# Performance work log

Hardware: AMD Instinct MI355X
Metric: run time of the kernel (lower is better)

## Reference

```python
import jax, jax.numpy as jnp
import numpy as np

N, E, F0, H = 100000, 3200000, 256, 128
TEMP = 2.0
ALPHA = 0.2  # leaky relu slope
EPS_BN = 1e-5
EPS_LN = 1e-5


def spmm(vals, row, col, X):
    # sparse [N,N] @ dense [N,D] via gather + segment_sum
    return jax.ops.segment_sum(vals[:, None] * X[col], row, num_segments=N)


def batchnorm(h, g, b):
    mu = jnp.mean(h, axis=0, keepdims=True)
    var = jnp.var(h, axis=0, keepdims=True)
    return (h - mu) * jax.lax.rsqrt(var + EPS_BN) * g + b


def layernorm(h, g, b):
    mu = jnp.mean(h, axis=-1, keepdims=True)
    var = jnp.var(h, axis=-1, keepdims=True)
    return (h - mu) * jax.lax.rsqrt(var + EPS_LN) * g + b


def setup_inputs() -> dict:
    key = jax.random.key(0)
    ks = jax.random.split(key, 32)
    x = jax.random.normal(ks[0], (N, F0), dtype=jnp.float32)
    edge_row = jax.random.randint(ks[1], (E,), 0, N)
    edge_col = jax.random.randint(ks[2], (E,), 0, N)
    adj_vals = jax.random.uniform(ks[3], (E,), dtype=jnp.float32) / 32.0  # ~normalized adj
    sf = lambda k, sh: jax.random.normal(k, sh, dtype=jnp.float32) * 0.05
    in_dim = 3 * F0 + 1
    return {
        "x": x, "edge_row": edge_row, "edge_col": edge_col, "adj_vals": adj_vals,
        # LowPassExtractor (GCN)
        "W_gc1": sf(ks[4], (F0, 2 * H)), "b_gc1": jnp.zeros((2 * H,), jnp.float32),
        "bn1_g": jnp.ones((2 * H,), jnp.float32), "bn1_b": jnp.zeros((2 * H,), jnp.float32),
        "W_gc2": sf(ks[5], (2 * H, H)), "b_gc2": jnp.zeros((H,), jnp.float32),
        "bn2_g": jnp.ones((H,), jnp.float32), "bn2_b": jnp.zeros((H,), jnp.float32),
        # Gating
        "Wg1": sf(ks[6], (in_dim, H)), "bg1": jnp.zeros((H,), jnp.float32),
        "ln_g": jnp.ones((H,), jnp.float32), "ln_b": jnp.zeros((H,), jnp.float32),
        "Wg2": sf(ks[7], (H, 2)), "bg2": jnp.zeros((2,), jnp.float32),
        # HighPassExpert
        "Wxp": sf(ks[8], (F0, H)), "bxp": jnp.zeros((H,), jnp.float32),
        "res_scale": jnp.asarray(1.0, jnp.float32),
        "rn_g": jnp.ones((H,), jnp.float32), "rn_b": jnp.zeros((H,), jnp.float32),
        "Wq": sf(ks[9], (H, H)), "Wk": sf(ks[10], (H, H)), "Wv": sf(ks[11], (H, H)),
    }


def reference(x, edge_row, edge_col, adj_vals,
              W_gc1, b_gc1, bn1_g, bn1_b, W_gc2, b_gc2, bn2_g, bn2_b,
              Wg1, bg1, ln_g, ln_b, Wg2, bg2,
              Wxp, bxp, res_scale, rn_g, rn_b, Wq, Wk, Wv):
    # ---- LowPassExtractor: two GCN layers (spmm(adj, xW)+b) with batchnorm+relu
    h1 = jax.nn.relu(batchnorm(spmm(adj_vals, edge_row, edge_col, x @ W_gc1) + b_gc1, bn1_g, bn1_b))
    low = jax.nn.relu(batchnorm(spmm(adj_vals, edge_row, edge_col, h1 @ W_gc2) + b_gc2, bn2_g, bn2_b))

    # ---- Gating: neighborhood stats via spmm
    AX = spmm(adj_vals, edge_row, edge_col, x)
    deg = jax.ops.segment_sum(adj_vals, edge_row, num_segments=N)[:, None]
    x_mean = AX / (deg + 1e-8)
    AX2 = spmm(adj_vals, edge_row, edge_col, x * x)
    var = AX2 / (deg + 1e-8) - x_mean * x_mean
    x_std = jnp.sqrt(jnp.clip(var, 0.0))
    x_cat = jnp.concatenate([x, AX - x, x_std, deg], axis=1)  # [N, 3*F0+1]
    hg = jax.nn.relu(layernorm(x_cat @ Wg1 + bg1, ln_g, ln_b))
    gate = jax.nn.softmax((hg @ Wg2 + bg2) / TEMP, axis=1)  # [N, 2]

    # ---- HighPassExpert: GAT-style sparse attention on normalized residual
    residual = layernorm(res_scale * (x @ Wxp + bxp - low), rn_g, rn_b)
    Q, K, V = residual @ Wq, residual @ Wk, residual @ Wv
    scores = jnp.sum(Q[edge_row] * K[edge_col], axis=1) / jnp.sqrt(jnp.float32(H))
    exp_s = jnp.exp(jnp.where(scores > 0, scores, ALPHA * scores))
    denom = jax.ops.segment_sum(exp_s, edge_row, num_segments=N)
    attn = exp_s / (denom[edge_row] + 1e-16)
    high = jax.ops.segment_sum(attn[:, None] * V[edge_col], edge_row, num_segments=N)

    output = gate[:, 0:1] * low + gate[:, 1:2] * high
    return output, gate, low, high
```

## Files before the change

kernel.cpp:

```cpp
#include <hip/hip_runtime.h>

#define F0 256
#define HD 128
#define NP 100352

typedef unsigned short u16;
typedef __attribute__((ext_vector_type(8))) short short8;
typedef __attribute__((ext_vector_type(4))) float f32x4;

__device__ inline float bf2f(u16 u) {
    union { unsigned int i; float f; } v; v.i = ((unsigned int)u) << 16; return v.f;
}
__device__ inline u16 f2bf(float f) {
    union { float f; unsigned int i; } v; v.f = f;
    unsigned int r = v.i + 0x7FFF + ((v.i >> 16) & 1);
    return (u16)(r >> 16);
}

#define GLOAD16(gp, lp) __builtin_amdgcn_global_load_lds( \
    (const __attribute__((address_space(1))) void*)(gp), \
    (__attribute__((address_space(3))) void*)(lp), 16, 0, 0)

__global__ void k_hist(const int* __restrict__ row, int* __restrict__ counts, int E) {
    int e = blockIdx.x * blockDim.x + threadIdx.x;
    if (e < E) atomicAdd(&counts[row[e]], 1);
}

__global__ void k_scan_blk(const int* __restrict__ counts, int* __restrict__ scan_out,
                           int* __restrict__ partials, int n) {
    __shared__ int wsum[16];
    int t = threadIdx.x;
    int i = blockIdx.x * 1024 + t;
    int v = (i < n) ? counts[i] : 0;
    int lane = t & 63, w = t >> 6;
    #pragma unroll
    for (int off = 1; off < 64; off <<= 1) { int u = __shfl_up(v, off); if (lane >= off) v += u; }
    if (lane == 63) wsum[w] = v;
    __syncthreads();
    if (t < 16) {
        int s = wsum[t];
        #pragma unroll
        for (int off = 1; off < 16; off <<= 1) { int u = __shfl_up(s, off); if (t >= off) s += u; }
        wsum[t] = s;
    }
    __syncthreads();
    int add = (w > 0) ? wsum[w - 1] : 0;
    if (i < n) scan_out[i] = v + add;
    if (t == 1023) partials[blockIdx.x] = wsum[15];
}

__global__ void k_scan_part(int* partials, int nb) {
    __shared__ int ws2[2];
    int t = threadIdx.x;
    int v = (t < nb) ? partials[t] : 0;
    int lane = t & 63, w = t >> 6;
    #pragma unroll
    for (int off = 1; off < 64; off <<= 1) { int u = __shfl_up(v, off); if (lane >= off) v += u; }
    if (lane == 63) ws2[w] = v;
    __syncthreads();
    if (w == 1) v += ws2[0];
    if (t < nb) partials[t] = v;
}

__global__ void k_scan_add(int* __restrict__ row_ptr, const int* __restrict__ partials, int n) {
    int b = blockIdx.x;
    int i = b * 1024 + threadIdx.x;
    if (b == 0 && threadIdx.x == 0) row_ptr[0] = 0;
    int add = (b > 0) ? partials[b - 1] : 0;
    if (i < n) row_ptr[1 + i] += add;
}

__global__ void k_scatter_cv(const int* __restrict__ row, const int* __restrict__ ecol,
                             const float* __restrict__ avals, const int* __restrict__ row_ptr,
                             int* __restrict__ cursor, int2* __restrict__ cv, int E) {
    int e = blockIdx.x * blockDim.x + threadIdx.x;
    if (e >= E) return;
    int r = row[e];
    int pos = row_ptr[r] + atomicAdd(&cursor[r], 1);
    cv[pos] = make_int2(ecol[e], __float_as_int(avals[e]));
}

__global__ void k_cast_x(const float* __restrict__ x, u16* __restrict__ xb, int total4) {
    int i = blockIdx.x * blockDim.x + threadIdx.x;
    if (i >= total4) return;
    float4 v = ((const float4*)x)[i];
    ((ushort4*)xb)[i] = make_ushort4(f2bf(v.x), f2bf(v.y), f2bf(v.z), f2bf(v.w));
}

__global__ void k_prep_w(const float* __restrict__ W_gc1, const float* __restrict__ W_gc2,
                         const float* __restrict__ Wg1, const float* __restrict__ Wxp,
                         const float* __restrict__ Wq, const float* __restrict__ Wk,
                         const float* __restrict__ Wv,
                         u16* Wgc1t, u16* Wgc2t, u16* Wdt, u16* W1t, u16* W2t,
                         u16* Wxpt, u16* Wqt, u16* Wkt, u16* Wvt) {
    int z = blockIdx.z;
    int idx = blockIdx.x * 256 + threadIdx.x;
    if (z == 0) { if (idx < 65536) { int n = idx >> 8, k = idx & 255; Wgc1t[idx] = f2bf(W_gc1[k * 256 + n]); } }
    else if (z == 1) { if (idx < 32768) { int n = idx >> 8, k = idx & 255; Wgc2t[idx] = f2bf(W_gc2[k * 128 + n]); } }
    else if (z == 2) { if (idx < 32768) { int n = idx >> 8, k = idx & 255; Wdt[idx] = f2bf(Wg1[k * 128 + n] - Wg1[(k + 256) * 128 + n]); } }
    else if (z == 3) { if (idx < 32768) { int n = idx >> 8, k = idx & 255; W1t[idx] = f2bf(Wg1[(k + 256) * 128 + n]); } }
    else if (z == 4) { if (idx < 32768) { int n = idx >> 8, k = idx & 255; W2t[idx] = f2bf(Wg1[(k + 512) * 128 + n]); } }
    else if (z == 5) { if (idx < 32768) { int n = idx >> 8, k = idx & 255; Wxpt[idx] = f2bf(Wxp[k * 128 + n]); } }
    else if (z == 6) { if (idx < 16384) { int n = idx >> 7, k = idx & 127; Wqt[idx] = f2bf(Wq[k * 128 + n]); } }
    else if (z == 7) { if (idx < 16384) { int n = idx >> 7, k = idx & 127; Wkt[idx] = f2bf(Wk[k * 128 + n]); } }
    else if (z == 8) { if (idx < 16384) { int n = idx >> 7, k = idx & 127; Wvt[idx] = f2bf(Wv[k * 128 + n]); } }
}

__global__ void k_spmm_x2(const u16* __restrict__ Xb, const int* __restrict__ row_ptr,
                          const int2* __restrict__ cv,
                          u16* __restrict__ AXb, u16* __restrict__ XSTDb,
                          float* __restrict__ deg, int N) {
    int wid = blockIdx.x * 4 + (threadIdx.x >> 6);
    if (wid >= N) return;
    int lane = threadIdx.x & 63;
    float a0 = 0, a1 = 0, a2 = 0, a3 = 0;
    float q0 = 0, q1 = 0, q2 = 0, q3 = 0, d = 0;
    int s = row_ptr[wid], e = row_ptr[wid + 1];
    int j = s;
    for (; j + 3 < e; j += 4) {
        int2 cc[4]; ushort4 xb[4];
        #pragma unroll
        for (int t = 0; t < 4; ++t) cc[t] = cv[j + t];
        #pragma unroll
        for (int t = 0; t < 4; ++t) xb[t] = *(const ushort4*)(Xb + (size_t)cc[t].x * F0 + lane * 4);
        #pragma unroll
        for (int t = 0; t < 4; ++t) {
            float x0 = bf2f(xb[t].x), x1 = bf2f(xb[t].y), x2 = bf2f(xb[t].z), x3 = bf2f(xb[t].w);
            float vv = __int_as_float(cc[t].y);
            a0 += vv * x0; a1 += vv * x1; a2 += vv * x2; a3 += vv * x3;
            q0 += vv * x0 * x0; q1 += vv * x1 * x1; q2 += vv * x2 * x2; q3 += vv * x3 * x3;
            d += vv;
        }
    }
    for (; j < e; ++j) {
        int2 cc = cv[j];
        float v0 = __int_as_float(cc.y);
        ushort4 xb0 = *(const ushort4*)(Xb + (size_t)cc.x * F0 + lane * 4);
        float x0 = bf2f(xb0.x), x1 = bf2f(xb0.y), x2 = bf2f(xb0.z), x3 = bf2f(xb0.w);
        a0 += v0 * x0; a1 += v0 * x1; a2 += v0 * x2; a3 += v0 * x3;
        q0 += v0 * x0 * x0; q1 += v0 * x1 * x1; q2 += v0 * x2 * x2; q3 += v0 * x3 * x3;
        d += v0;
    }
    float inv = 1.0f / (d + 1e-8f);
    float m0 = a0 * inv, m1 = a1 * inv, m2 = a2 * inv, m3 = a3 * inv;
    float s0 = sqrtf(fmaxf(q0 * inv - m0 * m0, 0.f));
    float s1 = sqrtf(fmaxf(q1 * inv - m1 * m1, 0.f));
    float s2 = sqrtf(fmaxf(q2 * inv - m2 * m2, 0.f));
    float s3 = sqrtf(fmaxf(q3 * inv - m3 * m3, 0.f));
    *(ushort4*)(AXb + (size_t)wid * F0 + lane * 4) = make_ushort4(f2bf(a0), f2bf(a1), f2bf(a2), f2bf(a3));
    *(ushort4*)(XSTDb + (size_t)wid * F0 + lane * 4) = make_ushort4(f2bf(s0), f2bf(s1), f2bf(s2), f2bf(s3));
    if (lane == 0) deg[wid] = d;
}

__global__ void k_spmm128(const u16* __restrict__ Xb, const int* __restrict__ row_ptr,
                          const int2* __restrict__ cv, u16* __restrict__ OUT, int N) {
    int wid = blockIdx.x * 4 + (threadIdx.x >> 6);
    if (wid >= N) return;
    int lane = threadIdx.x & 63;
    float a0 = 0, a1 = 0;
    int s = row_ptr[wid], e = row_ptr[wid + 1];
    int j = s;
    for (; j + 3 < e; j += 4) {
        int2 cc[4]; ushort2 xb[4];
        #pragma unroll
        for (int t = 0; t < 4; ++t) cc[t] = cv[j + t];
        #pragma unroll
        for (int t = 0; t < 4; ++t) xb[t] = *(const ushort2*)(Xb + (size_t)cc[t].x * HD + lane * 2);
        #pragma unroll
        for (int t = 0; t < 4; ++t) {
            float vv = __int_as_float(cc[t].y);
            a0 += vv * bf2f(xb[t].x); a1 += vv * bf2f(xb[t].y);
        }
    }
    for (; j < e; ++j) {
        int2 cc = cv[j];
        float v0 = __int_as_float(cc.y);
        ushort2 x0 = *(const ushort2*)(Xb + (size_t)cc.x * HD + lane * 2);
        a0 += v0 * bf2f(x0.x); a1 += v0 * bf2f(x0.y);
    }
    *(ushort2*)(OUT + (size_t)wid * HD + lane * 2) = make_ushort2(f2bf(a0), f2bf(a1));
}

__device__ inline void mm_core(const u16* __restrict__ A, const u16* __restrict__ Bt,
                               int K, int ldA, int ldB, int m0, int n0,
                               u16* As, u16* Bs, f32x4 acc[4][4]) {
    int t = threadIdx.x, w = t >> 6, l = t & 63;
    int wr = (w >> 1) * 64, wc = (w & 1) * 64;
    int aoff = (wr + (l & 15)) * 32 + (l >> 4) * 8;
    int boff = (wc + (l & 15)) * 32 + (l >> 4) * 8;
    for (int k0 = 0; k0 < K; k0 += 32) {
        __syncthreads();
        #pragma unroll
        for (int s = 0; s < 2; ++s) {
            int i = s * 256 + t;
            int row = i >> 2, ch = i & 3;
            GLOAD16(A + (size_t)(m0 + row) * ldA + k0 + ch * 8, As + i * 8);
            GLOAD16(Bt + (size_t)(n0 + row) * ldB + k0 + ch * 8, Bs + i * 8);
        }
        __syncthreads();
        short8 af[4], bfr[4];
        #pragma unroll
        for (int i = 0; i < 4; ++i) af[i] = *(const short8*)(As + aoff + i * 16 * 32);
        #pragma unroll
        for (int j = 0; j < 4; ++j) bfr[j] = *(const short8*)(Bs + boff + j * 16 * 32);
        #pragma unroll
        for (int i = 0; i < 4; ++i)
            #pragma unroll
            for (int j = 0; j < 4; ++j)
                acc[i][j] = __builtin_amdgcn_mfma_f32_16x16x32_bf16(af[i], bfr[j], acc[i][j], 0, 0, 0);
    }
}

__device__ inline void mm_zero(f32x4 acc[4][4]) {
    #pragma unroll
    for (int i = 0; i < 4; ++i)
        #pragma unroll
        for (int j = 0; j < 4; ++j)
            acc[i][j] = (f32x4){0.f, 0.f, 0.f, 0.f};
}

__global__ __launch_bounds__(256) void k_mm_f32(const u16* __restrict__ A, const u16* __restrict__ Bt,
                                                float* __restrict__ C, const float* __restrict__ bias,
                                                int M, int K, int Nc) {
    __shared__ __align__(16) u16 As[128 * 32];
    __shared__ __align__(16) u16 Bs[128 * 32];
    int m0 = blockIdx.x * 128, n0 = blockIdx.y * 128;
    f32x4 acc[4][4]; mm_zero(acc);
    mm_core(A, Bt, K, K, K, m0, n0, As, Bs, acc);
    int t = threadIdx.x, w = t >> 6, l = t & 63;
    int rbase = m0 + (w >> 1) * 64 + (l >> 4) * 4;
    int cbase = n0 + (w & 1) * 64 + (l & 15);
    #pragma unroll
    for (int j = 0; j < 4; ++j) {
        float bj = bias ? bias[cbase + j * 16] : 0.f;
        #pragma unroll
        for (int i = 0; i < 4; ++i)
            #pragma unroll
            for (int r = 0; r < 4; ++r) {
                int row = rbase + i * 16 + r;
                if (row < M) C[(size_t)row * Nc + cbase + j * 16] = acc[i][j][r] + bj;
            }
    }
}

__global__ __launch_bounds__(256) void k_mm_bf(const u16* __restrict__ A, const u16* __restrict__ Bt,
                                               u16* __restrict__ C, int M, int K, int Nc) {
    __shared__ __align__(16) u16 As[128 * 32];
    __shared__ __align__(16) u16 Bs[128 * 32];
    int m0 = blockIdx.x * 128, n0 = blockIdx.y * 128;
    f32x4 acc[4][4]; mm_zero(acc);
    mm_core(A, Bt, K, K, K, m0, n0, As, Bs, acc);
    int t = threadIdx.x, w = t >> 6, l = t & 63;
    int rbase = m0 + (w >> 1) * 64 + (l >> 4) * 4;
    int cbase = n0 + (w & 1) * 64 + (l & 15);
    #pragma unroll
    for (int j = 0; j < 4; ++j)
        #pragma unroll
        for (int i = 0; i < 4; ++i)
            #pragma unroll
            for (int r = 0; r < 4; ++r) {
                int row = rbase + i * 16 + r;
                if (row < M) C[(size_t)row * Nc + cbase + j * 16] = f2bf(acc[i][j][r]);
            }
}

__global__ __launch_bounds__(256) void k_mm_gate(const u16* A0, const u16* A1, const u16* A2,
                                                 const u16* B0, const u16* B1, const u16* B2,
                                                 float* __restrict__ C, const float* __restrict__ bg1,
                                                 const float* __restrict__ wlast,
                                                 const float* __restrict__ deg, int M) {
    __shared__ __align__(16) u16 As[128 * 32];
    __shared__ __align__(16) u16 Bs[128 * 32];
    int m0 = blockIdx.x * 128;
    f32x4 acc[4][4]; mm_zero(acc);
    mm_core(A0, B0, 256, 256, 256, m0, 0, As, Bs, acc);
    mm_core(A1, B1, 256, 256, 256, m0, 0, As, Bs, acc);
    mm_core(A2, B2, 256, 256, 256, m0, 0, As, Bs, acc);
    int t = threadIdx.x, w = t >> 6, l = t & 63;
    int rbase = m0 + (w >> 1) * 64 + (l >> 4) * 4;
    int cbase = (w & 1) * 64 + (l & 15);
    float wl[4], bg[4];
    #pragma unroll
    for (int j = 0; j < 4; ++j) { wl[j] = wlast[cbase + j * 16]; bg[j] = bg1[cbase + j * 16]; }
    float dg[4][4];
    #pragma unroll
    for (int i = 0; i < 4; ++i)
        #pragma unroll
        for (int r = 0; r < 4; ++r) {
            int row = rbase + i * 16 + r;
            dg[i][r] = (row < M) ? deg[row] : 0.f;
        }
    #pragma unroll
    for (int j = 0; j < 4; ++j)
        #pragma unroll
        for (int i = 0; i < 4; ++i)
            #pragma unroll
            for (int r = 0; r < 4; ++r) {
                int row = rbase + i * 16 + r;
                if (row < M) C[(size_t)row * 128 + cbase + j * 16] = acc[i][j][r] + bg[j] + dg[i][r] * wl[j];
            }
}

__global__ __launch_bounds__(256) void k_mm_qkv(const u16* __restrict__ A,
                                                const u16* Wqt, const u16* Wkt, const u16* Wvt,
                                                float* Q, u16* Kb, u16* Vb, int M) {
    __shared__ __align__(16) u16 As[128 * 32];
    __shared__ __align__(16) u16 Bs[128 * 32];
    int z = blockIdx.z;
    const u16* Bt = (z == 0) ? Wqt : (z == 1) ? Wkt : Wvt;
    int m0 = blockIdx.x * 128;
    f32x4 acc[4][4]; mm_zero(acc);
    mm_core(A, Bt, 128, 128, 128, m0, 0, As, Bs, acc);
    int t = threadIdx.x, w = t >> 6, l = t & 63;
    int rbase = m0 + (w >> 1) * 64 + (l >> 4) * 4;
    int cbase = (w & 1) * 64 + (l & 15);
    if (z == 0) {
        #pragma unroll
        for (int j = 0; j < 4; ++j)
            #pragma unroll
            for (int i = 0; i < 4; ++i)
                #pragma unroll
                for (int r = 0; r < 4; ++r) {
                    int row = rbase + i * 16 + r;
                    if (row < M) Q[(size_t)row * 128 + cbase + j * 16] = acc[i][j][r];
                }
    } else {
        u16* C = (z == 1) ? Kb : Vb;
        #pragma unroll
        for (int j = 0; j < 4; ++j)
            #pragma unroll
            for (int i = 0; i < 4; ++i)
                #pragma unroll
                for (int r = 0; r < 4; ++r) {
                    int row = rbase + i * 16 + r;
                    if (row < M) C[(size_t)row * 128 + cbase + j * 16] = f2bf(acc[i][j][r]);
                }
    }
}

__global__ void k_bn_stats_bf(const u16* __restrict__ H, double* __restrict__ stats, int N, int C) {
    int t = threadIdx.x;
    int rpt = 256 / C;
    int rsub = t / C;
    int col = t - rsub * C;
    double s = 0.0, q = 0.0;
    for (long r = (long)blockIdx.x * rpt + rsub; r < N; r += (long)gridDim.x * rpt) {
        float v = bf2f(H[(size_t)r * C + col]);
        s += v; q += (double)v * v;
    }
    __shared__ double sh_s[256], sh_q[256];
    sh_s[t] = s; sh_q[t] = q;
    __syncthreads();
    if (t < C) {
        for (int k = 1; k < rpt; ++k) { s += sh_s[t + k * C]; q += sh_q[t + k * C]; }
        atomicAdd(&stats[t], s);
        atomicAdd(&stats[C + t], q);
    }
}

__global__ void k_bn_fin(const double* __restrict__ stats, const float* __restrict__ g,
                         const float* __restrict__ b, float* __restrict__ scale,
                         float* __restrict__ shift, int C, double invN) {
    int t = threadIdx.x;
    if (t >= C) return;
    double mean = stats[t] * invN;
    double var = stats[C + t] * invN - mean * mean;
    float sc = (float)((double)g[t] / sqrt(var + 1e-5));
    scale[t] = sc;
    shift[t] = b[t] - (float)mean * sc;
}

__global__ void k_bn_relu_bb(const u16* __restrict__ in, u16* __restrict__ out,
                             const float* __restrict__ scale, const float* __restrict__ shift,
                             int total4, int cmask4) {
    int i = blockIdx.x * blockDim.x + threadIdx.x;
    if (i >= total4) return;
    int c4 = i & cmask4;
    ushort4 v = ((const ushort4*)in)[i];
    float4 sc = ((const float4*)scale)[c4];
    float4 sh = ((const float4*)shift)[c4];
    ((ushort4*)out)[i] = make_ushort4(
        f2bf(fmaxf(bf2f(v.x) * sc.x + sh.x, 0.f)), f2bf(fmaxf(bf2f(v.y) * sc.y + sh.y, 0.f)),
        f2bf(fmaxf(bf2f(v.z) * sc.z + sh.z, 0.f)), f2bf(fmaxf(bf2f(v.w) * sc.w + sh.w, 0.f)));
}

__global__ void k_bn_relu_bf(const u16* __restrict__ in, float* __restrict__ out,
                             const float* __restrict__ scale, const float* __restrict__ shift,
                             int total4, int cmask4) {
    int i = blockIdx.x * blockDim.x + threadIdx.x;
    if (i >= total4) return;
    int c4 = i & cmask4;
    ushort4 v = ((const ushort4*)in)[i];
    float4 sc = ((const float4*)scale)[c4];
    float4 sh = ((const float4*)shift)[c4];
    ((float4*)out)[i] = make_float4(
        fmaxf(bf2f(v.x) * sc.x + sh.x, 0.f), fmaxf(bf2f(v.y) * sc.y + sh.y, 0.f),
        fmaxf(bf2f(v.z) * sc.z + sh.z, 0.f), fmaxf(bf2f(v.w) * sc.w + sh.w, 0.f));
}

__global__ void k_ln_gate(const float* __restrict__ Hg, const float* __restrict__ g,
                          const float* __restrict__ b, const float* __restrict__ Wg2,
                          const float* __restrict__ bg2, float* __restrict__ gate, int N) {
    int wid = blockIdx.x * 4 + (threadIdx.x >> 6);
    if (wid >= N) return;
    int lane = threadIdx.x & 63;
    float2 h = *(const float2*)(Hg + (size_t)wid * HD + lane * 2);
    float s1 = h.x + h.y, s2 = h.x * h.x + h.y * h.y;
    #pragma unroll
    for (int off = 32; off > 0; off >>= 1) { s1 += __shfl_xor(s1, off); s2 += __shfl_xor(s2, off); }
    float mu = s1 * (1.f / 128.f);
    float var = s2 * (1.f / 128.f) - mu * mu;
    float is = 1.0f / sqrtf(var + 1e-5f);
    float2 gg = *(const float2*)(g + lane * 2);
    float2 bb = *(const float2*)(b + lane * 2);
    float y0 = fmaxf((h.x - mu) * is * gg.x + bb.x, 0.f);
    float y1 = fmaxf((h.y - mu) * is * gg.y + bb.y, 0.f);
    float4 w = ((const float4*)Wg2)[lane];
    float t0 = y0 * w.x + y1 * w.z;
    float t1 = y0 * w.y + y1 * w.w;
    #pragma unroll
    for (int off = 32; off > 0; off >>= 1) { t0 += __shfl_xor(t0, off); t1 += __shfl_xor(t1, off); }
    if (lane == 0) {
        t0 = (t0 + bg2[0]) * 0.5f;
        t1 = (t1 + bg2[1]) * 0.5f;
        float m = fmaxf(t0, t1);
        float e0 = __expf(t0 - m), e1 = __expf(t1 - m);
        float inv = 1.0f / (e0 + e1);
        gate[(size_t)wid * 2 + 0] = e0 * inv;
        gate[(size_t)wid * 2 + 1] = e1 * inv;
    }
}

__global__ void k_resid_ln(const float* __restrict__ R0, const float* __restrict__ low,
                           const float* __restrict__ g, const float* __restrict__ b,
                           const float* __restrict__ rs_ptr, u16* __restrict__ resid, int N) {
    int wid = blockIdx.x * 4 + (threadIdx.x >> 6);
    if (wid >= N) return;
    int lane = threadIdx.x & 63;
    float rs = rs_ptr[0];
    float2 a = *(const float2*)(R0 + (size_t)wid * HD + lane * 2);
    float2 l = *(const float2*)(low + (size_t)wid * HD + lane * 2);
    float h0 = rs * (a.x - l.x), h1 = rs * (a.y - l.y);
    float s1 = h0 + h1, s2 = h0 * h0 + h1 * h1;
    #pragma unroll
    for (int off = 32; off > 0; off >>= 1) { s1 += __shfl_xor(s1, off); s2 += __shfl_xor(s2, off); }
    float mu = s1 * (1.f / 128.f);
    float var = s2 * (1.f / 128.f) - mu * mu;
    float is = 1.0f / sqrtf(var + 1e-5f);
    float2 gg = *(const float2*)(g + lane * 2);
    float2 bb = *(const float2*)(b + lane * 2);
    float y0 = (h0 - mu) * is * gg.x + bb.x;
    float y1 = (h1 - mu) * is * gg.y + bb.y;
    *(ushort2*)(resid + (size_t)wid * HD + lane * 2) = make_ushort2(f2bf(y0), f2bf(y1));
}

__global__ void k_attn_aggr(const float* __restrict__ Q, const u16* __restrict__ Kb,
                            const u16* __restrict__ Vb, const int* __restrict__ row_ptr,
                            const int2* __restrict__ cv,
                            const float* __restrict__ gate, const float* __restrict__ low,
                            float* __restrict__ high, float* __restrict__ outp, int N) {
    int wid = blockIdx.x * 4 + (threadIdx.x >> 6);
    if (wid >= N) return;
    int lane = threadIdx.x & 63;
    float2 q = *(const float2*)(Q + (size_t)wid * HD + lane * 2);
    float n0 = 0, n1 = 0, den = 0;
    int s = row_ptr[wid], e = row_ptr[wid + 1];
    int j = s;
    for (; j + 3 < e; j += 4) {
        int c[4]; ushort2 kb[4], vb[4];
        #pragma unroll
        for (int t = 0; t < 4; ++t) c[t] = cv[j + t].x;
        #pragma unroll
        for (int t = 0; t < 4; ++t) kb[t] = *(const ushort2*)(Kb + (size_t)c[t] * HD + lane * 2);
        #pragma unroll
        for (int t = 0; t < 4; ++t) vb[t] = *(const ushort2*)(Vb + (size_t)c[t] * HD + lane * 2);
        float sc[4];
        #pragma unroll
        for (int t = 0; t < 4; ++t) sc[t] = q.x * bf2f(kb[t].x) + q.y * bf2f(kb[t].y);
        #pragma unroll
        for (int off = 32; off > 0; off >>= 1) {
            #pragma unroll
            for (int t = 0; t < 4; ++t) sc[t] += __shfl_xor(sc[t], off);
        }
        #pragma unroll
        for (int t = 0; t < 4; ++t) {
            float p = sc[t] * 0.08838834764831845f;
            float ls = p > 0.f ? p : 0.2f * p;
            float ex = __expf(ls);
            n0 += ex * bf2f(vb[t].x);
            n1 += ex * bf2f(vb[t].y);
            den += ex;
        }
    }
    for (; j < e; ++j) {
        int c0 = cv[j].x;
        ushort2 kb0 = *(const ushort2*)(Kb + (size_t)c0 * HD + lane * 2);
        ushort2 vb0 = *(const ushort2*)(Vb + (size_t)c0 * HD + lane * 2);
        float sc0 = q.x * bf2f(kb0.x) + q.y * bf2f(kb0.y);
        #pragma unroll
        for (int off = 32; off > 0; off >>= 1) sc0 += __shfl_xor(sc0, off);
        float p = sc0 * 0.08838834764831845f;
        float ls = p > 0.f ? p : 0.2f * p;
        float ex = __expf(ls);
        n0 += ex * bf2f(vb0.x); n1 += ex * bf2f(vb0.y); den += ex;
    }
    float inv = 1.0f / (den + 1e-16f);
    float h0 = n0 * inv, h1 = n1 * inv;
    *(float2*)(high + (size_t)wid * HD + lane * 2) = make_float2(h0, h1);
    float g0 = gate[(size_t)wid * 2 + 0], g1 = gate[(size_t)wid * 2 + 1];
    float2 lw = *(const float2*)(low + (size_t)wid * HD + lane * 2);
    *(float2*)(outp + (size_t)wid * HD + lane * 2) = make_float2(g0 * lw.x + g1 * h0, g0 * lw.y + g1 * h1);
}

extern "C" void kernel_launch(void* const* d_in, const int* in_sizes, int n_in,
                              void* d_out, int out_size, void* d_ws, size_t ws_size,
                              hipStream_t stream) {
    const float* x      = (const float*)d_in[0];
    const int*   erow   = (const int*)d_in[1];
    const int*   ecol   = (const int*)d_in[2];
    const float* avals  = (const float*)d_in[3];
    const float* W_gc1  = (const float*)d_in[4];
    const float* bn1_g  = (const float*)d_in[6];
    const float* bn1_b  = (const float*)d_in[7];
    const float* W_gc2  = (const float*)d_in[8];
    const float* bn2_g  = (const float*)d_in[10];
    const float* bn2_b  = (const float*)d_in[11];
    const float* Wg1    = (const float*)d_in[12];
    const float* bg1    = (const float*)d_in[13];
    const float* ln_g   = (const float*)d_in[14];
    const float* ln_b   = (const float*)d_in[15];
    const float* Wg2    = (const float*)d_in[16];
    const float* bg2    = (const float*)d_in[17];
    const float* Wxp    = (const float*)d_in[18];
    const float* bxp    = (const float*)d_in[19];
    const float* rscale = (const float*)d_in[20];
    const float* rn_g   = (const float*)d_in[21];
    const float* rn_b   = (const float*)d_in[22];
    const float* Wq     = (const float*)d_in[23];
    const float* Wk     = (const float*)d_in[24];
    const float* Wv     = (const float*)d_in[25];

    const int N = in_sizes[0] / F0;
    const int E = in_sizes[1];

    char* base = (char*)d_ws;
    size_t off = 0;
    auto carve = [&](size_t bytes) -> char* {
        char* p = base + off;
        off += (bytes + 255) & ~(size_t)255;
        return p;
    };
    double* stats  = (double*)carve(4096);
    float* scaleb  = (float*)carve(1024);
    float* shiftb  = (float*)carve(1024);
    int*   partials= (int*)carve(2048);
    u16* Wgc1t = (u16*)carve(65536 * 2);
    u16* Wgc2t = (u16*)carve(32768 * 2);
    u16* Wdt   = (u16*)carve(32768 * 2);
    u16* W1t   = (u16*)carve(32768 * 2);
    u16* W2t   = (u16*)carve(32768 * 2);
    u16* Wxpt  = (u16*)carve(32768 * 2);
    u16* Wqt   = (u16*)carve(16384 * 2);
    u16* Wkt   = (u16*)carve(16384 * 2);
    u16* Wvt   = (u16*)carve(16384 * 2);
    int*   row_ptr = (int*)carve((size_t)(N + 1) * 4);
    int*   cursor  = (int*)carve((size_t)N * 4);
    float* deg     = (float*)carve((size_t)N * 4);
    int2*  cv      = (int2*)carve((size_t)E * 8);
    u16*   x_bf    = (u16*)carve((size_t)NP * F0 * 2);
    u16*   kvb     = (u16*)carve((size_t)NP * HD * 2 * 2);
    u16*   AX_bf   = (u16*)carve((size_t)NP * F0 * 2);
    u16*   XSTD_bf = (u16*)carve((size_t)NP * F0 * 2);
    u16*   h1_bf   = (u16*)carve((size_t)NP * F0 * 2);
    float* BIG3    = (float*)carve((size_t)NP * HD * 4);
    u16*   G2_bf   = (u16*)carve((size_t)NP * HD * 2);
    float* M3      = (float*)carve((size_t)NP * HD * 4);
    (void)ws_size; (void)n_in; (void)out_size;

    u16*   Kb    = kvb;
    u16*   Vb    = kvb + (size_t)N * HD;
    u16*   S1_bf = h1_bf;
    u16*   S2_bf = (u16*)BIG3;
    u16*   resid_bf = h1_bf;

    float* out_o    = (float*)d_out;
    float* out_gate = out_o + (size_t)N * HD;
    float* out_low  = out_gate + (size_t)N * 2;
    float* out_high = out_low + (size_t)N * HD;

    const int eb  = (E + 255) / 256;
    const int wb  = (N + 3) / 4;
    const int NB1 = (N + 1023) / 1024;
    const int gx  = (N + 127) / 128;
    const dim3 blk(256);

    hipMemsetAsync(cursor, 0, (size_t)N * 4, stream);
    k_hist<<<eb, blk, 0, stream>>>(erow, cursor, E);
    k_scan_blk<<<NB1, 1024, 0, stream>>>(cursor, row_ptr + 1, partials, N);
    k_scan_part<<<1, 128, 0, stream>>>(partials, NB1);
    k_scan_add<<<NB1, 1024, 0, stream>>>(row_ptr, partials, N);
    hipMemsetAsync(cursor, 0, (size_t)N * 4, stream);
    k_scatter_cv<<<eb, blk, 0, stream>>>(erow, ecol, avals, row_ptr, cursor, cv, E);

    k_cast_x<<<(N * 64 + 255) / 256, blk, 0, stream>>>(x, x_bf, N * 64);
    k_prep_w<<<dim3(256, 1, 9), blk, 0, stream>>>(W_gc1, W_gc2, Wg1, Wxp, Wq, Wk, Wv,
                                                  Wgc1t, Wgc2t, Wdt, W1t, W2t, Wxpt, Wqt, Wkt, Wvt);

    k_spmm_x2<<<wb, blk, 0, stream>>>(x_bf, row_ptr, cv, AX_bf, XSTD_bf, deg, N);

    k_mm_bf<<<dim3(gx, 2), blk, 0, stream>>>(AX_bf, Wgc1t, S1_bf, N, 256, 256);
    hipMemsetAsync(stats, 0, 4096, stream);
    k_bn_stats_bf<<<1024, blk, 0, stream>>>(S1_bf, stats, N, 256);
    k_bn_fin<<<1, blk, 0, stream>>>(stats, bn1_g, bn1_b, scaleb, shiftb, 256, 1.0 / N);
    k_bn_relu_bb<<<(N * 64 + 255) / 256, blk, 0, stream>>>(S1_bf, h1_bf, scaleb, shiftb, N * 64, 63);
    k_mm_bf<<<dim3(gx, 1), blk, 0, stream>>>(h1_bf, Wgc2t, G2_bf, N, 256, 128);
    k_spmm128<<<wb, blk, 0, stream>>>(G2_bf, row_ptr, cv, S2_bf, N);
    hipMemsetAsync(stats, 0, 2048, stream);
    k_bn_stats_bf<<<1024, blk, 0, stream>>>(S2_bf, stats, N, 128);
    k_bn_fin<<<1, blk, 0, stream>>>(stats, bn2_g, bn2_b, scaleb, shiftb, 128, 1.0 / N);
    k_bn_relu_bf<<<(N * 32 + 255) / 256, blk, 0, stream>>>(S2_bf, out_low, scaleb, shiftb, N * 32, 31);

    k_mm_gate<<<dim3(gx, 1), blk, 0, stream>>>(x_bf, AX_bf, XSTD_bf, Wdt, W1t, W2t,
                                               M3, bg1, Wg1 + (size_t)768 * 128, deg, N);
    k_ln_gate<<<wb, blk, 0, stream>>>(M3, ln_g, ln_b, Wg2, bg2, out_gate, N);

    k_mm_f32<<<dim3(gx, 1), blk, 0, stream>>>(x_bf, Wxpt, BIG3, bxp, N, 256, 128);
    k_resid_ln<<<wb, blk, 0, stream>>>(BIG3, out_low, rn_g, rn_b, rscale, resid_bf, N);
    k_mm_qkv<<<dim3(gx, 1, 3), blk, 0, stream>>>(resid_bf, Wqt, Wkt, Wvt, M3, Kb, Vb, N);
    k_attn_aggr<<<wb, blk, 0, stream>>>(M3, Kb, Vb, row_ptr, cv, out_gate, out_low, out_high, out_o, N);
}
```

Before: 1.512 ms.

## Two-pass bucketed CSR scatter and 16-lane-per-edge attention score loads

The single random-scatter CSR build becomes two passes. First, edges are binned into 1024-row buckets using shared-memory histograms and a per-bucket global cursor, written to a temporary int4 buffer. Second, each edge is scattered to its final CSR slot from that bucket-ordered buffer, which should make the atomic and store traffic more local. Separately, the attention kernel now computes each of four edges' scores with 16 lanes using 16-byte K loads and a 4-step shuffle reduction instead of a 6-step full-wave reduction, at the cost of an extra pass over memory and reuse of the M3 workspace as scratch.

```diff
diff --git a/kernel.cpp b/kernel.cpp
--- a/kernel.cpp
+++ b/kernel.cpp
@@ -70,14 +70,51 @@
     if (i < n) row_ptr[1 + i] += add;
 }
 
-__global__ void k_scatter_cv(const int* __restrict__ row, const int* __restrict__ ecol,
-                             const float* __restrict__ avals, const int* __restrict__ row_ptr,
-                             int* __restrict__ cursor, int2* __restrict__ cv, int E) {
-    int e = blockIdx.x * blockDim.x + threadIdx.x;
-    if (e >= E) return;
-    int r = row[e];
-    int pos = row_ptr[r] + atomicAdd(&cursor[r], 1);
-    cv[pos] = make_int2(ecol[e], __float_as_int(avals[e]));
+__global__ void k_binit(const int* __restrict__ row_ptr, int* __restrict__ bcursor, int nb) {
+    int b = blockIdx.x * 256 + threadIdx.x;
+    if (b < nb) bcursor[b] = row_ptr[b << 10];
+}
+
+__global__ __launch_bounds__(256) void k_bucketA(const int* __restrict__ erow,
+                                                 const int* __restrict__ ecol,
+                                                 const float* __restrict__ avals,
+                                                 int* __restrict__ bcursor,
+                                                 int4* __restrict__ tmp, int E, int nb) {
+    __shared__ int hcnt[128];
+    __shared__ int hbase[128];
+    int t = threadIdx.x;
+    for (int i = t; i < nb; i += 256) hcnt[i] = 0;
+    __syncthreads();
+    int start = blockIdx.x * 2048;
+    int r[8], c[8]; float v[8]; int loc[8];
+    #pragma unroll
+    for (int k = 0; k < 8; ++k) {
+        int e = start + k * 256 + t;
+        bool ok = e < E;
+        r[k] = ok ? erow[e] : -1;
+        c[k] = ok ? ecol[e] : 0;
+        v[k] = ok ? avals[e] : 0.f;
+        loc[k] = (r[k] >= 0) ? atomicAdd(&hcnt[r[k] >> 10], 1) : 0;
+    }
+    __syncthreads();
+    for (int i = t; i < nb; i += 256) hbase[i] = atomicAdd(&bcursor[i], hcnt[i]);
+    __syncthreads();
+    #pragma unroll
+    for (int k = 0; k < 8; ++k) {
+        if (r[k] >= 0) {
+            int b = r[k] >> 10;
+            tmp[(size_t)hbase[b] + loc[k]] = make_int4(r[k], c[k], __float_as_int(v[k]), 0);
+        }
+    }
+}
+
+__global__ void k_bucketB(const int4* __restrict__ tmp, const int* __restrict__ row_ptr,
+                          int* __restrict__ cursor, int2* __restrict__ cv, int E) {
+    for (int e = blockIdx.x * 256 + threadIdx.x; e < E; e += gridDim.x * 256) {
+        int4 tt = tmp[e];
+        int pos = row_ptr[tt.x] + atomicAdd(&cursor[tt.x], 1);
+        cv[pos] = make_int2(tt.y, tt.z);
+    }
 }
 
 __global__ void k_cast_x(const float* __restrict__ x, u16* __restrict__ xb, int total4) {
@@ -462,41 +499,49 @@
     int wid = blockIdx.x * 4 + (threadIdx.x >> 6);
     if (wid >= N) return;
     int lane = threadIdx.x & 63;
-    float2 q = *(const float2*)(Q + (size_t)wid * HD + lane * 2);
+    int sub = lane & 15;
+    int g = lane >> 4;
+    float qs[8];
+    {
+        const float4* qp = (const float4*)(Q + (size_t)wid * HD + sub * 8);
+        float4 q0 = qp[0], q1 = qp[1];
+        qs[0] = q0.x; qs[1] = q0.y; qs[2] = q0.z; qs[3] = q0.w;
+        qs[4] = q1.x; qs[5] = q1.y; qs[6] = q1.z; qs[7] = q1.w;
+    }
+    float2 qv = *(const float2*)(Q + (size_t)wid * HD + lane * 2);
     float n0 = 0, n1 = 0, den = 0;
     int s = row_ptr[wid], e = row_ptr[wid + 1];
     int j = s;
     for (; j + 3 < e; j += 4) {
-        int c[4]; ushort2 kb[4], vb[4];
-        #pragma unroll
-        for (int t = 0; t < 4; ++t) c[t] = cv[j + t].x;
-        #pragma unroll
-        for (int t = 0; t < 4; ++t) kb[t] = *(const ushort2*)(Kb + (size_t)c[t] * HD + lane * 2);
-        #pragma unroll
-        for (int t = 0; t < 4; ++t) vb[t] = *(const ushort2*)(Vb + (size_t)c[t] * HD + lane * 2);
-        float sc[4];
-        #pragma unroll
-        for (int t = 0; t < 4; ++t) sc[t] = q.x * bf2f(kb[t].x) + q.y * bf2f(kb[t].y);
-        #pragma unroll
-        for (int off = 32; off > 0; off >>= 1) {
-            #pragma unroll
-            for (int t = 0; t < 4; ++t) sc[t] += __shfl_xor(sc[t], off);
-        }
+        int cg = cv[j + g].x;
+        short8 kk = *(const short8*)(Kb + (size_t)cg * HD + sub * 8);
+        float p = qs[0] * bf2f((u16)kk[0]) + qs[1] * bf2f((u16)kk[1])
+                + qs[2] * bf2f((u16)kk[2]) + qs[3] * bf2f((u16)kk[3])
+                + qs[4] * bf2f((u16)kk[4]) + qs[5] * bf2f((u16)kk[5])
+                + qs[6] * bf2f((u16)kk[6]) + qs[7] * bf2f((u16)kk[7]);
+        p += __shfl_xor(p, 1); p += __shfl_xor(p, 2);
+        p += __shfl_xor(p, 4); p += __shfl_xor(p, 8);
+        float sc = p * 0.08838834764831845f;
+        float ls = sc > 0.f ? sc : 0.2f * sc;
+        float ex = __expf(ls);
+        float exb[4]; int cb[4];
+        #pragma unroll
+        for (int t = 0; t < 4; ++t) { exb[t] = __shfl(ex, t << 4); cb[t] = __shfl(cg, t << 4); }
+        ushort2 vb[4];
+        #pragma unroll
+        for (int t = 0; t < 4; ++t) vb[t] = *(const ushort2*)(Vb + (size_t)cb[t] * HD + lane * 2);
         #pragma unroll
         for (int t = 0; t < 4; ++t) {
-            float p = sc[t] * 0.08838834764831845f;
-            float ls = p > 0.f ? p : 0.2f * p;
-            float ex = __expf(ls);
-            n0 += ex * bf2f(vb[t].x);
-            n1 += ex * bf2f(vb[t].y);
-            den += ex;
+            n0 += exb[t] * bf2f(vb[t].x);
+            n1 += exb[t] * bf2f(vb[t].y);
+            den += exb[t];
         }
     }
     for (; j < e; ++j) {
         int c0 = cv[j].x;
         ushort2 kb0 = *(const ushort2*)(Kb + (size_t)c0 * HD + lane * 2);
         ushort2 vb0 = *(const ushort2*)(Vb + (size_t)c0 * HD + lane * 2);
-        float sc0 = q.x * bf2f(kb0.x) + q.y * bf2f(kb0.y);
+        float sc0 = qv.x * bf2f(kb0.x) + qv.y * bf2f(kb0.y);
         #pragma unroll
         for (int off = 32; off > 0; off >>= 1) sc0 += __shfl_xor(sc0, off);
         float p = sc0 * 0.08838834764831845f;
@@ -554,6 +599,7 @@
     float* scaleb  = (float*)carve(1024);
     float* shiftb  = (float*)carve(1024);
     int*   partials= (int*)carve(2048);
+    int*   bcursor = (int*)carve(512);
     u16* Wgc1t = (u16*)carve(65536 * 2);
     u16* Wgc2t = (u16*)carve(32768 * 2);
     u16* Wdt   = (u16*)carve(32768 * 2);
@@ -582,6 +628,7 @@
     u16*   S1_bf = h1_bf;
     u16*   S2_bf = (u16*)BIG3;
     u16*   resid_bf = h1_bf;
+    int4*  tmp   = (int4*)M3;
 
     float* out_o    = (float*)d_out;
     float* out_gate = out_o + (size_t)N * HD;
@@ -591,6 +638,7 @@
     const int eb  = (E + 255) / 256;
     const int wb  = (N + 3) / 4;
     const int NB1 = (N + 1023) / 1024;
+    const int nb  = (N + 1023) >> 10;
     const int gx  = (N + 127) / 128;
     const dim3 blk(256);
 
@@ -599,8 +647,10 @@
     k_scan_blk<<<NB1, 1024, 0, stream>>>(cursor, row_ptr + 1, partials, N);
     k_scan_part<<<1, 128, 0, stream>>>(partials, NB1);
     k_scan_add<<<NB1, 1024, 0, stream>>>(row_ptr, partials, N);
+    k_binit<<<1, blk, 0, stream>>>(row_ptr, bcursor, nb);
+    k_bucketA<<<(E + 2047) / 2048, blk, 0, stream>>>(erow, ecol, avals, bcursor, tmp, E, nb);
     hipMemsetAsync(cursor, 0, (size_t)N * 4, stream);
-    k_scatter_cv<<<eb, blk, 0, stream>>>(erow, ecol, avals, row_ptr, cursor, cv, E);
+    k_bucketB<<<2048, blk, 0, stream>>>(tmp, row_ptr, cursor, cv, E);
 
     k_cast_x<<<(N * 64 + 255) / 256, blk, 0, stream>>>(x, x_bf, N * 64);
     k_prep_w<<<dim3(256, 1, 9), blk, 0, stream>>>(W_gc1, W_gc2, Wg1, Wxp, Wq, Wk, Wv,
```

New measurement: 1.549 ms. 1.02x slower.
